# Kernel optimization log

Measured on AMD Instinct MI355X. Metric: run time of the kernel, lower is better.

Reference implementation:

```python
import jax, jax.numpy as jnp
import numpy as np

VOCAB = 10000
HID = 256

def setup_inputs() -> dict:
    key = jax.random.key(0)
    ks = jax.random.split(key, 7)
    B, T = 64, 64
    input_data = jax.random.randint(ks[0], (B, T), 0, VOCAB, dtype=jnp.int32)
    targets = jax.random.randint(ks[1], (B, T), 0, VOCAB, dtype=jnp.int32)
    # Xavier-ish scaled params
    E = jax.random.normal(ks[2], (VOCAB, HID), dtype=jnp.float32) * (1.0 / np.sqrt(HID))
    W_lstm = jax.random.normal(ks[3], (2 * HID, 4 * HID), dtype=jnp.float32) * (1.0 / np.sqrt(2 * HID))
    b_lstm = jnp.zeros((4 * HID,), dtype=jnp.float32)
    W_dense = jax.random.normal(ks[4], (HID, VOCAB), dtype=jnp.float32) * (1.0 / np.sqrt(HID))
    b_dense = jnp.zeros((VOCAB,), dtype=jnp.float32)
    return {"input_data": input_data, "targets": targets, "E": E,
            "W_lstm": W_lstm, "b_lstm": b_lstm, "W_dense": W_dense, "b_dense": b_dense}

def lstm_scan(xs, W, b, h0, c0):
    # xs: [T, B, H] time-major. TF LSTMCell: gates = [x,h]@W + b, order i,j,f,o, forget_bias=1.0
    def step(carry, x):
        h, c = carry
        gates = jnp.concatenate([x, h], axis=-1) @ W + b  # [B, 4H]
        i, j, f, o = jnp.split(gates, 4, axis=-1)
        c_new = jax.nn.sigmoid(f + 1.0) * c + jax.nn.sigmoid(i) * jnp.tanh(j)
        h_new = jax.nn.sigmoid(o) * jnp.tanh(c_new)
        return (h_new, c_new), h_new
    (hT, cT), hs = jax.lax.scan(step, (h0, c0), xs)
    return hs, (hT, cT)

def reference(input_data, targets, E, W_lstm, b_lstm, W_dense, b_dense):
    B, T = input_data.shape
    inputs = E[input_data]                       # [B, T, H] embedding lookup (no dropout: eval)
    xs = jnp.transpose(inputs, (1, 0, 2))        # [T, B, H]
    h0 = jnp.zeros((B, HID), dtype=E.dtype)
    c0 = jnp.zeros((B, HID), dtype=E.dtype)
    hs, _ = lstm_scan(xs, W_lstm, b_lstm, h0, c0)  # [T, B, H]
    outputs = jnp.transpose(hs, (1, 0, 2))       # [B, T, H]
    logits = outputs @ W_dense + b_dense         # [B, T, V]
    logp = jax.nn.log_softmax(logits, axis=-1)
    ce = -jnp.take_along_axis(logp, targets[..., None].astype(jnp.int32), axis=-1)[..., 0]  # [B, T]
    perplexity = jnp.exp(ce)                     # elementwise, as in add_loss_op
    return perplexity
```

## Files before the change

### kernel.cpp

```cpp
#include <hip/hip_runtime.h>
#include <math.h>

#define VOCABN 10000
#define HIDN   256
#define GATES  1024
#define BN     64
#define TN     64
#define BT     4096
#define NCT    625

typedef unsigned int       u32;
typedef unsigned short     u16;
typedef unsigned long long u64;
typedef float v4f __attribute__((ext_vector_type(4)));
typedef short v8s __attribute__((ext_vector_type(8)));

#define SENT 0xFFFFFFFFFFFFFFFFULL

__device__ __forceinline__ float bf2f(u16 u) {
    return __uint_as_float(((u32)u) << 16);
}
__device__ __forceinline__ u16 f2bf(float f) {
    u32 u = __float_as_uint(f);
    u += 0x7FFFu + ((u >> 16) & 1u);
    return (u16)(u >> 16);
}
__device__ __forceinline__ float fast_sigmoid(float x) {
    return 1.0f / (1.0f + __expf(-x));
}
__device__ __forceinline__ float fast_tanh(float x) {
    float e = __expf(-2.0f * fabsf(x));
    float t = (1.0f - e) / (1.0f + e);
    return copysignf(t, x);
}
__device__ __forceinline__ u64 llc_load(const u64* p) {
    return __hip_atomic_load(p, __ATOMIC_RELAXED, __HIP_MEMORY_SCOPE_AGENT);
}
__device__ __forceinline__ void llc_store(u64* p, u64 v) {
    __hip_atomic_store(p, v, __ATOMIC_RELAXED, __HIP_MEMORY_SCOPE_AGENT);
}

__device__ __forceinline__ void wfrag_dev(
    const float* __restrict__ src, u16* __restrict__ dst, int ncols, int c,
    int t, u16 lt[HIDN][16])
{
    const float* s = src + (size_t)t * ncols + c * 16;
    #pragma unroll
    for (int j4 = 0; j4 < 4; ++j4) {
        float4 v = *(const float4*)(s + j4 * 4);
        lt[t][j4*4+0] = f2bf(v.x);
        lt[t][j4*4+1] = f2bf(v.y);
        lt[t][j4*4+2] = f2bf(v.z);
        lt[t][j4*4+3] = f2bf(v.w);
    }
    __syncthreads();
    #pragma unroll
    for (int h = 0; h < 2; ++h) {
        int f = t + h * 256;
        int q = f >> 6, l = f & 63;
        int m = l & 15, kb = q * 32 + ((l >> 4) & 3) * 8;
        u32 w[4];
        #pragma unroll
        for (int j = 0; j < 4; ++j)
            w[j] = (u32)lt[kb + 2*j][m] | ((u32)lt[kb + 2*j + 1][m] << 16);
        *(uint4*)(dst + (((size_t)c * 8 + q) * 64 + l) * 8) =
            make_uint4(w[0], w[1], w[2], w[3]);
    }
}

__global__ __launch_bounds__(256) void k_wfrag2(
    const float* __restrict__ W_lstm,
    u16* __restrict__ Wxf, u16* __restrict__ Whf,
    u64* __restrict__ Hx64)
{
    __shared__ u16 lt[HIDN][16];
    const int bid = blockIdx.x;
    if (bid < 64) {
        Hx64[(size_t)bid * 256 + threadIdx.x] = SENT;
        wfrag_dev(W_lstm, Wxf, GATES, bid, threadIdx.x, lt);
    } else {
        wfrag_dev(W_lstm + (size_t)HIDN * GATES, Whf, GATES, bid - 64,
                  threadIdx.x, lt);
    }
}

__global__ __launch_bounds__(256) void k_wfrag3(
    const float* __restrict__ W_lstm,
    const float* __restrict__ W_dense,
    u16* __restrict__ Wxf, u16* __restrict__ Whf, u16* __restrict__ Wf,
    u64* __restrict__ Hx64)
{
    __shared__ u16 lt[HIDN][16];
    const int bid = blockIdx.x;
    if (bid < 64) {
        Hx64[(size_t)bid * 256 + threadIdx.x] = SENT;
        wfrag_dev(W_lstm, Wxf, GATES, bid, threadIdx.x, lt);
    } else if (bid < 128) {
        wfrag_dev(W_lstm + (size_t)HIDN * GATES, Whf, GATES, bid - 64,
                  threadIdx.x, lt);
    } else {
        wfrag_dev(W_dense, Wf, VOCABN, bid - 128, threadIdx.x, lt);
    }
}

__global__ __launch_bounds__(256) void k_wfrag(
    const float* __restrict__ src,
    u16*         __restrict__ dst,
    int ncols)
{
    __shared__ u16 lt[HIDN][16];
    wfrag_dev(src, dst, ncols, blockIdx.x, threadIdx.x, lt);
}

__global__ __launch_bounds__(256) void k_xgates(
    const int*   __restrict__ idx,
    const float* __restrict__ E,
    const u16*   __restrict__ Wxf,
    const float* __restrict__ bl,
    float*       __restrict__ gx)
{
    const int r0   = blockIdx.x * 16;
    const int tid  = threadIdx.x;
    const int w    = tid >> 6, lane = tid & 63;
    const int m    = lane & 15, quad = lane >> 4;

    v8s a[8];
    {
        const float* e = E + (size_t)idx[r0 + m] * HIDN + quad * 8;
        #pragma unroll
        for (int q = 0; q < 8; ++q) {
            float4 x0 = *(const float4*)(e + q * 32);
            float4 x1 = *(const float4*)(e + q * 32 + 4);
            uint4 t4 = make_uint4(
                (u32)f2bf(x0.x) | ((u32)f2bf(x0.y) << 16),
                (u32)f2bf(x0.z) | ((u32)f2bf(x0.w) << 16),
                (u32)f2bf(x1.x) | ((u32)f2bf(x1.y) << 16),
                (u32)f2bf(x1.z) | ((u32)f2bf(x1.w) << 16));
            a[q] = *(v8s*)&t4;
        }
    }

    for (int c = w; c < GATES / 16; c += 4) {
        v4f acc = {0.f, 0.f, 0.f, 0.f};
        #pragma unroll
        for (int q = 0; q < 8; ++q) {
            v8s b = *(const v8s*)(Wxf + (((size_t)c * 8 + q) * 64 + lane) * 8);
            acc = __builtin_amdgcn_mfma_f32_16x16x32_bf16(a[q], b, acc, 0, 0, 0);
        }
        const int col = c * 16 + m;
        const float bv = bl[col];
        #pragma unroll
        for (int r = 0; r < 4; ++r)
            gx[(size_t)(r0 + quad * 4 + r) * GATES + col] = acc[r] + bv;
    }
}

__global__ __launch_bounds__(256) void k_plstm(
    const u16*   __restrict__ Whf,
    const float* __restrict__ gx,
    u16*                      Hx,
    u16*         __restrict__ Hb)
{
    __shared__ uint4 Wl4[4 * 512];
    __shared__ float gl[2][4][16][16];

    const int tid  = threadIdx.x;
    const int rg   = blockIdx.x >> 4;
    const int ns   = blockIdx.x & 15;
    const int u0   = ns * 16;
    const int w    = tid >> 6;
    const int lane = tid & 63;
    const int m    = lane & 15, kq = lane >> 4;

    {
        const uint4* src = (const uint4*)Whf;
        #pragma unroll
        for (int i = 0; i < 8; ++i) {
            int e  = tid + i * 256;
            int ct = e >> 9, off = e & 511;
            Wl4[e] = src[(size_t)(ct * 16 + ns) * 512 + off];
        }
    }
    {
        float* g0 = (float*)gl[0];
        #pragma unroll
        for (int j = 0; j < 4; ++j) g0[tid * 4 + j] = 0.0f;
    }
    __syncthreads();

    const u16* Wl = (const u16*)Wl4;

    const int r = tid >> 4, u = tid & 15;
    const int b = rg * 16 + r;
    const float* gxp = gx + (size_t)b * TN * GATES + u0 + u;
    u16* hbp = Hb + (size_t)b * TN * HIDN + u0 + u;
    const int hxw = b * HIDN + u0 + u;
    const int aoff = (rg * 16 + m) * HIDN + kq * 8;
    u64* const hx64 = (u64*)Hx;
    const int cidx = (rg * 16 + (tid >> 2)) * (HIDN / 4) + ns * 4 + (tid & 3);

    float cstate = 0.0f;
    float4 gxr;
    gxr.x = gxp[0]; gxr.y = gxp[256]; gxr.z = gxp[512]; gxr.w = gxp[768];

    for (int t = 0; t < TN; ++t) {
        float4 gxn = gxr;
        if (t + 1 < TN) {
            const float* p = gxp + (size_t)(t + 1) * GATES;
            gxn.x = p[0]; gxn.y = p[256]; gxn.z = p[512]; gxn.w = p[768];
        }

        if (t + 1 < TN && tid < 64)
            llc_store(hx64 + (size_t)((t + 1) & 3) * (BN * HIDN / 4) + cidx,
                      SENT);

        if (t > 0) {
            const u64* hsrc =
                (const u64*)(Hx + (size_t)((t - 1) & 3) * (BN * HIDN) + aoff);
            u64 d[16];
            #pragma unroll
            for (int q = 0; q < 8; ++q) {
                d[2 * q]     = llc_load(hsrc + q * 8);
                d[2 * q + 1] = llc_load(hsrc + q * 8 + 1);
            }
            #pragma unroll
            for (int i = 0; i < 16; ++i)
                while (d[i] == SENT)
                    d[i] = llc_load(hsrc + (i >> 1) * 8 + (i & 1));

            v4f acc = {0.f, 0.f, 0.f, 0.f};
            #pragma unroll
            for (int q = 0; q < 8; ++q) {
                union { u64 dd[2]; v8s v; } av;
                av.dd[0] = d[2 * q];
                av.dd[1] = d[2 * q + 1];
                v8s bf = *(const v8s*)(Wl + ((w * 8 + q) * 64 + lane) * 8);
                acc = __builtin_amdgcn_mfma_f32_16x16x32_bf16(av.v, bf, acc,
                                                              0, 0, 0);
            }
            #pragma unroll
            for (int rr = 0; rr < 4; ++rr)
                gl[t & 1][w][kq * 4 + rr][m] = acc[rr];
        }
        __syncthreads();

        {
            float ai = gl[t & 1][0][r][u] + gxr.x;
            float aj = gl[t & 1][1][r][u] + gxr.y;
            float af = gl[t & 1][2][r][u] + gxr.z;
            float ao = gl[t & 1][3][r][u] + gxr.w;
            float ig = fast_sigmoid(ai);
            float fg = fast_sigmoid(af + 1.0f);
            float og = fast_sigmoid(ao);
            float jt = fast_tanh(aj);
            cstate = fg * cstate + ig * jt;
            float hn = og * fast_tanh(cstate);
            u32 hv = f2bf(hn);
            hbp[(size_t)t * HIDN] = (u16)hv;

            if (t + 1 < TN) {
                u32 p1 = __shfl_down(hv, 1);
                u32 p2 = __shfl_down(hv, 2);
                u32 p3 = __shfl_down(hv, 3);
                if ((tid & 3) == 0) {
                    u64 pk = (u64)(hv | (p1 << 16))
                           | ((u64)(p2 | (p3 << 16)) << 32);
                    u64* dst =
                        (u64*)(Hx + (size_t)(t & 3) * (BN * HIDN) + hxw);
                    llc_store(dst, pk);
                }
            }
        }
        gxr = gxn;
    }
}

__global__ __launch_bounds__(256, 1) void k_dense(
    const u16*   __restrict__ Hb,
    const u16*   __restrict__ Wf,
    const float* __restrict__ bd,
    float*       __restrict__ S)
{
    __shared__ float Sl[64];
    const int bid = blockIdx.x;
    const int hv  = bid & 7;
    const int rg  = bid >> 3;
    const int r0  = rg * 64;
    const int tid = threadIdx.x;
    const int w   = tid >> 6, lane = tid & 63;
    const int m   = lane & 15, kq = lane >> 4;

    if (tid < 64) Sl[tid] = 0.0f;

    v8s a[4][8];
    #pragma unroll
    for (int rt = 0; rt < 4; ++rt) {
        const u16* hrow = Hb + (size_t)(r0 + rt * 16 + m) * HIDN + kq * 8;
        #pragma unroll
        for (int q = 0; q < 8; ++q)
            a[rt][q] = *(const v8s*)(hrow + q * 32);
    }
    __syncthreads();

    float s[4][4] = {{0.f,0.f,0.f,0.f},{0.f,0.f,0.f,0.f},
                     {0.f,0.f,0.f,0.f},{0.f,0.f,0.f,0.f}};
    const int cbeg = (hv * NCT) >> 3;
    const int cend = ((hv + 1) * NCT) >> 3;
    for (int c = cbeg + w; c < cend; c += 4) {
        v4f acc[4] = {{0.f,0.f,0.f,0.f},{0.f,0.f,0.f,0.f},
                      {0.f,0.f,0.f,0.f},{0.f,0.f,0.f,0.f}};
        #pragma unroll
        for (int q = 0; q < 8; ++q) {
            v8s bq = *(const v8s*)(Wf + (((size_t)c * 8 + q) * 64 + lane) * 8);
            #pragma unroll
            for (int rt = 0; rt < 4; ++rt)
                acc[rt] = __builtin_amdgcn_mfma_f32_16x16x32_bf16(
                              a[rt][q], bq, acc[rt], 0, 0, 0);
        }
        const float bv = bd[c * 16 + m];
        #pragma unroll
        for (int rt = 0; rt < 4; ++rt)
            #pragma unroll
            for (int r = 0; r < 4; ++r)
                s[rt][r] += __expf(acc[rt][r] + bv);
    }

    #pragma unroll
    for (int rt = 0; rt < 4; ++rt)
        #pragma unroll
        for (int r = 0; r < 4; ++r)
            atomicAdd(&Sl[rt * 16 + kq * 4 + r], s[rt][r]);
    __syncthreads();
    if (tid < 64) S[(size_t)hv * BT + r0 + tid] = Sl[tid];
}

__global__ __launch_bounds__(256) void k_target(
    const u16*   __restrict__ Hb,
    const u16*   __restrict__ Wf,
    const float* __restrict__ bd,
    const int*   __restrict__ tgt,
    const float* __restrict__ S,
    float*       __restrict__ out)
{
    const int tid = threadIdx.x;
    const int row = blockIdx.x * 8 + (tid >> 5);
    const int t   = tid & 31;
    const int q   = t >> 2, lq = t & 3;
    const int v   = tgt[row];
    const int c   = v >> 4, vm = v & 15;
    const int kb  = q * 32 + lq * 8;

    v8s h  = *(const v8s*)(Hb + (size_t)row * HIDN + kb);
    v8s wv = *(const v8s*)(Wf + (((size_t)c * 8 + q) * 64 + lq * 16 + vm) * 8);
    float acc = 0.0f;
    #pragma unroll
    for (int j = 0; j < 8; ++j)
        acc = fmaf(bf2f((u16)h[j]), bf2f((u16)wv[j]), acc);
    #pragma unroll
    for (int off = 16; off >= 1; off >>= 1)
        acc += __shfl_down(acc, off, 32);
    if (t == 0) {
        float tlv = acc + bd[v];
        float sum = 0.0f;
        #pragma unroll
        for (int p = 0; p < 8; ++p) sum += S[(size_t)p * BT + row];
        out[row] = __expf(__logf(sum) - tlv);
    }
}

extern "C" void kernel_launch(void* const* d_in, const int* in_sizes, int n_in,
                              void* d_out, int out_size, void* d_ws, size_t ws_size,
                              hipStream_t stream) {
    const int*   input   = (const int*)  d_in[0];
    const int*   targets = (const int*)  d_in[1];
    const float* E       = (const float*)d_in[2];
    const float* W_lstm  = (const float*)d_in[3];
    const float* b_lstm  = (const float*)d_in[4];
    const float* W_dense = (const float*)d_in[5];
    const float* b_dense = (const float*)d_in[6];
    float* out = (float*)d_out;

    char* ws = (char*)d_ws;
    const bool wide = (ws_size >= ((size_t)25 << 20));

    if (wide) {
        float* gx  = (float*)ws;
        u16*   Wf  = (u16*)(ws + ((size_t)16 << 20));
        u16*   Hb  = (u16*)(ws + ((size_t)21 << 20) + ((size_t)256 << 10));
        u16*   Whf = (u16*)(ws + ((size_t)23 << 20) + ((size_t)256 << 10));
        u16*   Wxf = (u16*)(ws + ((size_t)23 << 20) + ((size_t)768 << 10));
        u16*   Hx  = (u16*)(ws + ((size_t)24 << 20) + ((size_t)256 << 10));
        float* S   = (float*)(ws + ((size_t)24 << 20) + ((size_t)384 << 10));

        k_wfrag3<<<753,     256, 0, stream>>>(W_lstm, W_dense, Wxf, Whf, Wf,
                                              (u64*)Hx);
        k_xgates<<<BT / 16, 256, 0, stream>>>(input, E, Wxf, b_lstm, gx);
        k_plstm <<<64,      256, 0, stream>>>(Whf, gx, Hx, Hb);
        k_dense <<<512,     256, 0, stream>>>(Hb, Wf, b_dense, S);
        k_target<<<BT / 8,  256, 0, stream>>>(Hb, Wf, b_dense, targets, S, out);
    } else {
        float* gx  = (float*)ws;
        u16*   Wf  = (u16*)ws;
        u16*   Hb  = (u16*)(ws + ((size_t)16 << 20));
        u16*   Whf = (u16*)(ws + ((size_t)18 << 20));
        u16*   Wxf = (u16*)(ws + ((size_t)18 << 20) + ((size_t)512 << 10));
        u16*   Hx  = (u16*)(ws + ((size_t)19 << 20));
        float* S   = (float*)(ws + ((size_t)19 << 20) + ((size_t)128 << 10));

        k_wfrag2<<<128,     256, 0, stream>>>(W_lstm, Wxf, Whf, (u64*)Hx);
        k_xgates<<<BT / 16, 256, 0, stream>>>(input, E, Wxf, b_lstm, gx);
        k_plstm <<<64,      256, 0, stream>>>(Whf, gx, Hx, Hb);
        k_wfrag <<<NCT,     256, 0, stream>>>(W_dense, Wf, VOCABN);
        k_dense <<<512,     256, 0, stream>>>(Hb, Wf, b_dense, S);
        k_target<<<BT / 8,  256, 0, stream>>>(Hb, Wf, b_dense, targets, S, out);
    }
}
```

Baseline: 407.9 us.

## Run LSTM recurrence per batch group in one block, dropping cross-block handoff

The recurrent LSTM kernel moves from 64 blocks, which passed hidden state through global memory with sentinel polling, to 4 blocks that each own a 16-row batch group and compute all 1024 gate columns themselves. Recurrent weights are held mostly in registers, with one quarter in a large dynamic LDS buffer, and the hidden state is double-buffered in LDS so each step needs only a workgroup barrier. The input-gate precompute now writes bf16 in a layout matched to the MFMA fragments to cut traffic. The cost is far less parallelism (4 CUs doing 16x more MFMA work each), very high register pressure, and bf16 rounding of the gate preactivations.

```diff
diff --git a/kernel.cpp b/kernel.cpp
--- a/kernel.cpp
+++ b/kernel.cpp
@@ -9,14 +9,17 @@
 #define BT     4096
 #define NCT    625
 
+#define HPITCH 264
+#define HBUFE  4224
+#define WLDS_B 131072
+#define SMEMSZ (WLDS_B + 2 * HBUFE * 2)
+
 typedef unsigned int       u32;
 typedef unsigned short     u16;
 typedef unsigned long long u64;
 typedef float v4f __attribute__((ext_vector_type(4)));
 typedef short v8s __attribute__((ext_vector_type(8)));
 
-#define SENT 0xFFFFFFFFFFFFFFFFULL
-
 __device__ __forceinline__ float bf2f(u16 u) {
     return __uint_as_float(((u32)u) << 16);
 }
@@ -32,12 +35,6 @@
     float e = __expf(-2.0f * fabsf(x));
     float t = (1.0f - e) / (1.0f + e);
     return copysignf(t, x);
-}
-__device__ __forceinline__ u64 llc_load(const u64* p) {
-    return __hip_atomic_load(p, __ATOMIC_RELAXED, __HIP_MEMORY_SCOPE_AGENT);
-}
-__device__ __forceinline__ void llc_store(u64* p, u64 v) {
-    __hip_atomic_store(p, v, __ATOMIC_RELAXED, __HIP_MEMORY_SCOPE_AGENT);
 }
 
 __device__ __forceinline__ void wfrag_dev(
@@ -70,37 +67,31 @@
 
 __global__ __launch_bounds__(256) void k_wfrag2(
     const float* __restrict__ W_lstm,
-    u16* __restrict__ Wxf, u16* __restrict__ Whf,
-    u64* __restrict__ Hx64)
+    u16* __restrict__ Wxf, u16* __restrict__ Whf)
 {
     __shared__ u16 lt[HIDN][16];
     const int bid = blockIdx.x;
-    if (bid < 64) {
-        Hx64[(size_t)bid * 256 + threadIdx.x] = SENT;
+    if (bid < 64)
         wfrag_dev(W_lstm, Wxf, GATES, bid, threadIdx.x, lt);
-    } else {
+    else
         wfrag_dev(W_lstm + (size_t)HIDN * GATES, Whf, GATES, bid - 64,
                   threadIdx.x, lt);
-    }
 }
 
 __global__ __launch_bounds__(256) void k_wfrag3(
     const float* __restrict__ W_lstm,
     const float* __restrict__ W_dense,
-    u16* __restrict__ Wxf, u16* __restrict__ Whf, u16* __restrict__ Wf,
-    u64* __restrict__ Hx64)
+    u16* __restrict__ Wxf, u16* __restrict__ Whf, u16* __restrict__ Wf)
 {
     __shared__ u16 lt[HIDN][16];
     const int bid = blockIdx.x;
-    if (bid < 64) {
-        Hx64[(size_t)bid * 256 + threadIdx.x] = SENT;
+    if (bid < 64)
         wfrag_dev(W_lstm, Wxf, GATES, bid, threadIdx.x, lt);
-    } else if (bid < 128) {
+    else if (bid < 128)
         wfrag_dev(W_lstm + (size_t)HIDN * GATES, Whf, GATES, bid - 64,
                   threadIdx.x, lt);
-    } else {
+    else
         wfrag_dev(W_dense, Wf, VOCABN, bid - 128, threadIdx.x, lt);
-    }
 }
 
 __global__ __launch_bounds__(256) void k_wfrag(
@@ -117,16 +108,18 @@
     const float* __restrict__ E,
     const u16*   __restrict__ Wxf,
     const float* __restrict__ bl,
-    float*       __restrict__ gx)
-{
-    const int r0   = blockIdx.x * 16;
-    const int tid  = threadIdx.x;
-    const int w    = tid >> 6, lane = tid & 63;
-    const int m    = lane & 15, quad = lane >> 4;
+    u64*         __restrict__ gx2)
+{
+    const int bid = blockIdx.x;
+    const int t   = bid >> 2, rg = bid & 3;
+    const int tid = threadIdx.x;
+    const int w   = tid >> 6, lane = tid & 63;
+    const int m   = lane & 15, quad = lane >> 4;
 
     v8s a[8];
     {
-        const float* e = E + (size_t)idx[r0 + m] * HIDN + quad * 8;
+        const float* e = E + (size_t)idx[(rg * 16 + m) * TN + t] * HIDN
+                         + quad * 8;
         #pragma unroll
         for (int q = 0; q < 8; ++q) {
             float4 x0 = *(const float4*)(e + q * 32);
@@ -140,139 +133,156 @@
         }
     }
 
-    for (int c = w; c < GATES / 16; c += 4) {
+    for (int i = 0; i < 16; ++i) {
+        const int c = 4 * i + w;
         v4f acc = {0.f, 0.f, 0.f, 0.f};
         #pragma unroll
         for (int q = 0; q < 8; ++q) {
             v8s b = *(const v8s*)(Wxf + (((size_t)c * 8 + q) * 64 + lane) * 8);
             acc = __builtin_amdgcn_mfma_f32_16x16x32_bf16(a[q], b, acc, 0, 0, 0);
         }
-        const int col = c * 16 + m;
-        const float bv = bl[col];
-        #pragma unroll
-        for (int r = 0; r < 4; ++r)
-            gx[(size_t)(r0 + quad * 4 + r) * GATES + col] = acc[r] + bv;
-    }
-}
-
-__global__ __launch_bounds__(256) void k_plstm(
+        const float bv = bl[c * 16 + m];
+        u32 lo = (u32)f2bf(acc[0] + bv) | ((u32)f2bf(acc[1] + bv) << 16);
+        u32 hi = (u32)f2bf(acc[2] + bv) | ((u32)f2bf(acc[3] + bv) << 16);
+        u64 pk = (u64)lo | ((u64)hi << 32);
+        const size_t di =
+            ((((size_t)t * 4 + rg) * 4 + ((c & 15) >> 2)) * 64 + lane) * 16
+            + (c & 3) * 4 + (c >> 4);
+        gx2[di] = pk;
+    }
+}
+
+__global__ __launch_bounds__(256, 1) void k_plstm(
     const u16*   __restrict__ Whf,
-    const float* __restrict__ gx,
-    u16*                      Hx,
+    const u64*   __restrict__ gx2,
     u16*         __restrict__ Hb)
 {
-    __shared__ uint4 Wl4[4 * 512];
-    __shared__ float gl[2][4][16][16];
+    extern __shared__ char smem[];
+    u16* WgL   = (u16*)smem;
+    u16* hbufu = (u16*)(smem + WLDS_B);
 
     const int tid  = threadIdx.x;
-    const int rg   = blockIdx.x >> 4;
-    const int ns   = blockIdx.x & 15;
-    const int u0   = ns * 16;
+    const int rg   = blockIdx.x;
     const int w    = tid >> 6;
     const int lane = tid & 63;
     const int m    = lane & 15, kq = lane >> 4;
 
+    v8s wr[3][4][8];
+    #pragma unroll
+    for (int gg = 0; gg < 3; ++gg)
+        #pragma unroll
+        for (int gm = 0; gm < 4; ++gm)
+            #pragma unroll
+            for (int q = 0; q < 8; ++q)
+                wr[gg][gm][q] = *(const v8s*)(
+                    Whf + (((size_t)(gm * 16 + 4 * w + gg) * 8 + q) * 64
+                           + lane) * 8);
+
+    #pragma unroll
+    for (int gm = 0; gm < 4; ++gm)
+        #pragma unroll
+        for (int q = 0; q < 8; ++q)
+            *(uint4*)(WgL + ((w * 32 + gm * 8 + q) * 64 + lane) * 8) =
+                *(const uint4*)(
+                    Whf + (((size_t)(gm * 16 + 4 * w + 3) * 8 + q) * 64
+                           + lane) * 8);
+
     {
-        const uint4* src = (const uint4*)Whf;
-        #pragma unroll
-        for (int i = 0; i < 8; ++i) {
-            int e  = tid + i * 256;
-            int ct = e >> 9, off = e & 511;
-            Wl4[e] = src[(size_t)(ct * 16 + ns) * 512 + off];
-        }
-    }
+        u32* hz = (u32*)hbufu;
+        for (int i = tid; i < HBUFE; i += 256) hz[i] = 0u;
+    }
+
+    u64 gb[16];
     {
-        float* g0 = (float*)gl[0];
-        #pragma unroll
-        for (int j = 0; j < 4; ++j) g0[tid * 4 + j] = 0.0f;
-    }
+        const u64* g0 = gx2 + (((size_t)0 * 4 + rg) * 4 + w) * 64 * 16
+                        + (size_t)lane * 16;
+        #pragma unroll
+        for (int s = 0; s < 16; ++s) gb[s] = g0[s];
+    }
+
+    float cs[16];
+    #pragma unroll
+    for (int i = 0; i < 16; ++i) cs[i] = 0.0f;
+
     __syncthreads();
 
-    const u16* Wl = (const u16*)Wl4;
-
-    const int r = tid >> 4, u = tid & 15;
-    const int b = rg * 16 + r;
-    const float* gxp = gx + (size_t)b * TN * GATES + u0 + u;
-    u16* hbp = Hb + (size_t)b * TN * HIDN + u0 + u;
-    const int hxw = b * HIDN + u0 + u;
-    const int aoff = (rg * 16 + m) * HIDN + kq * 8;
-    u64* const hx64 = (u64*)Hx;
-    const int cidx = (rg * 16 + (tid >> 2)) * (HIDN / 4) + ns * 4 + (tid & 3);
-
-    float cstate = 0.0f;
-    float4 gxr;
-    gxr.x = gxp[0]; gxr.y = gxp[256]; gxr.z = gxp[512]; gxr.w = gxp[768];
+    #define CELL(GG, E0, E1, E2, E3)                                          \
+    {                                                                         \
+        _Pragma("unroll")                                                     \
+        for (int r = 0; r < 4; ++r) {                                         \
+            float xi = bf2f((u16)(gb[(GG)*4 + 0] >> (16 * r)));               \
+            float xj = bf2f((u16)(gb[(GG)*4 + 1] >> (16 * r)));               \
+            float xf = bf2f((u16)(gb[(GG)*4 + 2] >> (16 * r)));               \
+            float xo = bf2f((u16)(gb[(GG)*4 + 3] >> (16 * r)));               \
+            float ig = fast_sigmoid(E0[r] + xi);                              \
+            float jt = fast_tanh   (E1[r] + xj);                              \
+            float fg = fast_sigmoid(E2[r] + xf + 1.0f);                       \
+            float og = fast_sigmoid(E3[r] + xo);                              \
+            float cn = fg * cs[(GG)*4 + r] + ig * jt;                         \
+            cs[(GG)*4 + r] = cn;                                              \
+            u16 hv = f2bf(og * fast_tanh(cn));                                \
+            hwr[(kq * 4 + r) * HPITCH + (4 * w + (GG)) * 16 + m] = hv;        \
+            Hb[((size_t)(rg * 16 + kq * 4 + r) * TN + t) * HIDN              \
+               + (4 * w + (GG)) * 16 + m] = hv;                               \
+        }                                                                     \
+    }
+
+    #define PREFETCH_G(GG)                                                    \
+    if (t + 1 < TN) {                                                         \
+        const u64* gp = gx2 + ((((size_t)(t + 1) * 4 + rg) * 4 + w) * 64      \
+                               + lane) * 16 + (GG) * 4;                       \
+        gb[(GG)*4 + 0] = gp[0]; gb[(GG)*4 + 1] = gp[1];                       \
+        gb[(GG)*4 + 2] = gp[2]; gb[(GG)*4 + 3] = gp[3];                       \
+    }
 
     for (int t = 0; t < TN; ++t) {
-        float4 gxn = gxr;
-        if (t + 1 < TN) {
-            const float* p = gxp + (size_t)(t + 1) * GATES;
-            gxn.x = p[0]; gxn.y = p[256]; gxn.z = p[512]; gxn.w = p[768];
-        }
-
-        if (t + 1 < TN && tid < 64)
-            llc_store(hx64 + (size_t)((t + 1) & 3) * (BN * HIDN / 4) + cidx,
-                      SENT);
-
-        if (t > 0) {
-            const u64* hsrc =
-                (const u64*)(Hx + (size_t)((t - 1) & 3) * (BN * HIDN) + aoff);
-            u64 d[16];
+        const u16* hrd = hbufu + (t & 1) * HBUFE;
+        u16*       hwr = hbufu + ((t + 1) & 1) * HBUFE;
+
+        v8s a[8];
+        #pragma unroll
+        for (int q = 0; q < 8; ++q)
+            a[q] = *(const v8s*)(hrd + m * HPITCH + q * 32 + kq * 8);
+
+        #pragma unroll
+        for (int gg = 0; gg < 3; ++gg) {
+            v4f e0 = {0.f,0.f,0.f,0.f}, e1 = {0.f,0.f,0.f,0.f};
+            v4f e2 = {0.f,0.f,0.f,0.f}, e3 = {0.f,0.f,0.f,0.f};
             #pragma unroll
             for (int q = 0; q < 8; ++q) {
-                d[2 * q]     = llc_load(hsrc + q * 8);
-                d[2 * q + 1] = llc_load(hsrc + q * 8 + 1);
+                e0 = __builtin_amdgcn_mfma_f32_16x16x32_bf16(a[q], wr[gg][0][q], e0, 0, 0, 0);
+                e1 = __builtin_amdgcn_mfma_f32_16x16x32_bf16(a[q], wr[gg][1][q], e1, 0, 0, 0);
+                e2 = __builtin_amdgcn_mfma_f32_16x16x32_bf16(a[q], wr[gg][2][q], e2, 0, 0, 0);
+                e3 = __builtin_amdgcn_mfma_f32_16x16x32_bf16(a[q], wr[gg][3][q], e3, 0, 0, 0);
             }
-            #pragma unroll
-            for (int i = 0; i < 16; ++i)
-                while (d[i] == SENT)
-                    d[i] = llc_load(hsrc + (i >> 1) * 8 + (i & 1));
-
-            v4f acc = {0.f, 0.f, 0.f, 0.f};
+            CELL(gg, e0, e1, e2, e3)
+            PREFETCH_G(gg)
+        }
+
+        {
+            const u16* wl = WgL + w * 16384;
+            v4f e0 = {0.f,0.f,0.f,0.f}, e1 = {0.f,0.f,0.f,0.f};
+            v4f e2 = {0.f,0.f,0.f,0.f}, e3 = {0.f,0.f,0.f,0.f};
             #pragma unroll
             for (int q = 0; q < 8; ++q) {
-                union { u64 dd[2]; v8s v; } av;
-                av.dd[0] = d[2 * q];
-                av.dd[1] = d[2 * q + 1];
-                v8s bf = *(const v8s*)(Wl + ((w * 8 + q) * 64 + lane) * 8);
-                acc = __builtin_amdgcn_mfma_f32_16x16x32_bf16(av.v, bf, acc,
-                                                              0, 0, 0);
+                v8s b0 = *(const v8s*)(wl + ((0 * 8 + q) * 64 + lane) * 8);
+                v8s b1 = *(const v8s*)(wl + ((1 * 8 + q) * 64 + lane) * 8);
+                v8s b2 = *(const v8s*)(wl + ((2 * 8 + q) * 64 + lane) * 8);
+                v8s b3 = *(const v8s*)(wl + ((3 * 8 + q) * 64 + lane) * 8);
+                e0 = __builtin_amdgcn_mfma_f32_16x16x32_bf16(a[q], b0, e0, 0, 0, 0);
+                e1 = __builtin_amdgcn_mfma_f32_16x16x32_bf16(a[q], b1, e1, 0, 0, 0);
+                e2 = __builtin_amdgcn_mfma_f32_16x16x32_bf16(a[q], b2, e2, 0, 0, 0);
+                e3 = __builtin_amdgcn_mfma_f32_16x16x32_bf16(a[q], b3, e3, 0, 0, 0);
             }
-            #pragma unroll
-            for (int rr = 0; rr < 4; ++rr)
-                gl[t & 1][w][kq * 4 + rr][m] = acc[rr];
+            CELL(3, e0, e1, e2, e3)
+            PREFETCH_G(3)
         }
-        __syncthreads();
-
-        {
-            float ai = gl[t & 1][0][r][u] + gxr.x;
-            float aj = gl[t & 1][1][r][u] + gxr.y;
-            float af = gl[t & 1][2][r][u] + gxr.z;
-            float ao = gl[t & 1][3][r][u] + gxr.w;
-            float ig = fast_sigmoid(ai);
-            float fg = fast_sigmoid(af + 1.0f);
-            float og = fast_sigmoid(ao);
-            float jt = fast_tanh(aj);
-            cstate = fg * cstate + ig * jt;
-            float hn = og * fast_tanh(cstate);
-            u32 hv = f2bf(hn);
-            hbp[(size_t)t * HIDN] = (u16)hv;
-
-            if (t + 1 < TN) {
-                u32 p1 = __shfl_down(hv, 1);
-                u32 p2 = __shfl_down(hv, 2);
-                u32 p3 = __shfl_down(hv, 3);
-                if ((tid & 3) == 0) {
-                    u64 pk = (u64)(hv | (p1 << 16))
-                           | ((u64)(p2 | (p3 << 16)) << 32);
-                    u64* dst =
-                        (u64*)(Hx + (size_t)(t & 3) * (BN * HIDN) + hxw);
-                    llc_store(dst, pk);
-                }
-            }
-        }
-        gxr = gxn;
-    }
+
+        asm volatile("s_waitcnt lgkmcnt(0)" ::: "memory");
+        __builtin_amdgcn_s_barrier();
+    }
+    #undef CELL
+    #undef PREFETCH_G
 }
 
 __global__ __launch_bounds__(256, 1) void k_dense(
@@ -380,36 +390,41 @@
     const float* b_dense = (const float*)d_in[6];
     float* out = (float*)d_out;
 
+    static bool attr_done = false;
+    if (!attr_done) {
+        hipFuncSetAttribute((const void*)k_plstm,
+                            hipFuncAttributeMaxDynamicSharedMemorySize,
+                            SMEMSZ);
+        attr_done = true;
+    }
+
     char* ws = (char*)d_ws;
     const bool wide = (ws_size >= ((size_t)25 << 20));
 
     if (wide) {
-        float* gx  = (float*)ws;
+        u64*   gx2 = (u64*)ws;
         u16*   Wf  = (u16*)(ws + ((size_t)16 << 20));
         u16*   Hb  = (u16*)(ws + ((size_t)21 << 20) + ((size_t)256 << 10));
         u16*   Whf = (u16*)(ws + ((size_t)23 << 20) + ((size_t)256 << 10));
         u16*   Wxf = (u16*)(ws + ((size_t)23 << 20) + ((size_t)768 << 10));
-        u16*   Hx  = (u16*)(ws + ((size_t)24 << 20) + ((size_t)256 << 10));
         float* S   = (float*)(ws + ((size_t)24 << 20) + ((size_t)384 << 10));
 
-        k_wfrag3<<<753,     256, 0, stream>>>(W_lstm, W_dense, Wxf, Whf, Wf,
-                                              (u64*)Hx);
-        k_xgates<<<BT / 16, 256, 0, stream>>>(input, E, Wxf, b_lstm, gx);
-        k_plstm <<<64,      256, 0, stream>>>(Whf, gx, Hx, Hb);
+        k_wfrag3<<<753,     256, 0, stream>>>(W_lstm, W_dense, Wxf, Whf, Wf);
+        k_xgates<<<BT / 16, 256, 0, stream>>>(input, E, Wxf, b_lstm, gx2);
+        k_plstm <<<4,       256, SMEMSZ, stream>>>(Whf, gx2, Hb);
         k_dense <<<512,     256, 0, stream>>>(Hb, Wf, b_dense, S);
         k_target<<<BT / 8,  256, 0, stream>>>(Hb, Wf, b_dense, targets, S, out);
     } else {
-        float* gx  = (float*)ws;
+        u64*   gx2 = (u64*)ws;
         u16*   Wf  = (u16*)ws;
         u16*   Hb  = (u16*)(ws + ((size_t)16 << 20));
         u16*   Whf = (u16*)(ws + ((size_t)18 << 20));
         u16*   Wxf = (u16*)(ws + ((size_t)18 << 20) + ((size_t)512 << 10));
-        u16*   Hx  = (u16*)(ws + ((size_t)19 << 20));
         float* S   = (float*)(ws + ((size_t)19 << 20) + ((size_t)128 << 10));
 
-        k_wfrag2<<<128,     256, 0, stream>>>(W_lstm, Wxf, Whf, (u64*)Hx);
-        k_xgates<<<BT / 16, 256, 0, stream>>>(input, E, Wxf, b_lstm, gx);
-        k_plstm <<<64,      256, 0, stream>>>(Whf, gx, Hx, Hb);
+        k_wfrag2<<<128,     256, 0, stream>>>(W_lstm, Wxf, Whf);
+        k_xgates<<<BT / 16, 256, 0, stream>>>(input, E, Wxf, b_lstm, gx2);
+        k_plstm <<<4,       256, SMEMSZ, stream>>>(Whf, gx2, Hb);
         k_wfrag <<<NCT,     256, 0, stream>>>(W_dense, Wf, VOCABN);
         k_dense <<<512,     256, 0, stream>>>(Hb, Wf, b_dense, S);
         k_target<<<BT / 8,  256, 0, stream>>>(Hb, Wf, b_dense, targets, S, out);
```

New measurement: 490.2 us. 1.2x slower.
